# Optimization experiments

Hardware: AMD Instinct MI355X
Metric: run time of the kernel (lower is better)

The kernel has to match this reference:

```python
import jax, jax.numpy as jnp
import numpy as np

H = 512  # hidden_size
D = 512  # embed_dim == input_size
V = 50000  # embed_num
B, S = 64, 256
C = 5  # class_num


def setup_inputs() -> dict:
    key = jax.random.key(0)
    ks = jax.random.split(key, 8)
    sc_in = 1.0 / np.sqrt(D + H)
    return {
        "x": jax.random.randint(ks[0], (B, S), 0, V),
        "embed": jax.random.normal(ks[1], (V, D), dtype=jnp.float32) * 0.02,
        # gate order: [f, i, c, o]; each gate Linear(D+H -> H)
        "fwd_W": jax.random.normal(ks[2], (4, H, D + H), dtype=jnp.float32) * sc_in,
        "fwd_b": jax.random.normal(ks[3], (4, H), dtype=jnp.float32) * sc_in,
        "bwd_W": jax.random.normal(ks[4], (4, H, D + H), dtype=jnp.float32) * sc_in,
        "bwd_b": jax.random.normal(ks[5], (4, H), dtype=jnp.float32) * sc_in,
        "Wout": jax.random.normal(ks[6], (C, H), dtype=jnp.float32) * (1.0 / np.sqrt(H)),
        "bout": jax.random.normal(ks[7], (C,), dtype=jnp.float32) * 0.01,
    }


def _lstm_scan(xs, W, b):
    # xs: [S, B, D]; W: [4, H, D+H]; b: [4, H]
    Bsz = xs.shape[1]
    h0 = jnp.zeros((Bsz, H), xs.dtype)
    c0 = jnp.zeros((Bsz, H), xs.dtype)

    def step(carry, xt):
        h, c = carry
        z = jnp.concatenate([xt, h], axis=1)              # [B, D+H]
        gates = jnp.einsum('bk,ghk->gbh', z, W) + b[:, None, :]  # [4, B, H]
        f = jax.nn.sigmoid(gates[0])
        i = jax.nn.sigmoid(gates[1])
        ctil = jnp.tanh(gates[2])
        o = jax.nn.sigmoid(gates[3])
        # faithful to source: ct = f*ctil + i*ctil (prev cell state unused)
        c_new = (f + i) * ctil
        h_new = o * jnp.tanh(c_new)
        return (h_new, c_new), h_new

    _, hs = jax.lax.scan(step, (h0, c0), xs)
    return hs  # [S, B, H]


def reference(x, embed, fwd_W, fwd_b, bwd_W, bwd_b, Wout, bout):
    xe = embed[x]                      # [B, S, D]
    xs = jnp.transpose(xe, (1, 0, 2))  # [S, B, D]
    h_fwd = _lstm_scan(xs, fwd_W, fwd_b)                        # [S, B, H]
    h_bwd = _lstm_scan(xs[::-1], bwd_W, bwd_b)[::-1]            # aligned [S, B, H]
    combined = h_fwd * h_bwd           # elementwise product, per source
    pooled = jnp.max(jnp.tanh(combined), axis=0)  # max over time -> [B, H]
    return pooled @ Wout.T + bout      # [B, C]
```

## Files before the change

### kernel.cpp

```cpp
#include <hip/hip_runtime.h>
#include <math.h>

#define HH 512
#define DD 512
#define BB 64
#define SS 256
#define KK 1024
#define CC 5

typedef __attribute__((ext_vector_type(8))) short short8;
typedef __attribute__((ext_vector_type(4))) float float4v;

#define OFF_XEF     0u
#define OFF_HSPL    33554432u
#define OFF_FLG     34078720u
#define OFF_HIST    34079744u
#define OFF_POOLED  OFF_HSPL
#define HSPL_PLANE  131072

__device__ __forceinline__ unsigned f2bf_bits(float f) {
    unsigned u = __builtin_bit_cast(unsigned, f);
    return (u + 0x7fffu + ((u >> 16) & 1u)) >> 16;
}
__device__ __forceinline__ float sigm_(float v) {
    return 1.f / (1.f + expf(-v));
}
__device__ __forceinline__ float tanh_(float v) {
    return tanhf(v);
}

__global__ __launch_bounds__(256)
void gather_split_k(const int* __restrict__ x, const float* __restrict__ embed,
                    short* __restrict__ xef)
{
    const int s   = blockIdx.x;
    const int tid = threadIdx.x;
    const int b   = tid & 63;
    const int seg = tid >> 6;
    __shared__ int rows[BB];
    if (tid < BB) rows[tid] = x[tid * SS + s];
    __syncthreads();
    const float* e = embed + (size_t)rows[b] * DD + seg * 128;
    short* oh = xef + ((size_t)(s * 2 + 0) * BB + b) * 512 + seg * 128;
    short* ol = xef + ((size_t)(s * 2 + 1) * BB + b) * 512 + seg * 128;
    for (int k0 = 0; k0 < 128; k0 += 8) {
        const float4 a = *(const float4*)(e + k0);
        const float4 c = *(const float4*)(e + k0 + 4);
        const float ev[8] = {a.x, a.y, a.z, a.w, c.x, c.y, c.z, c.w};
        short8 vh, vl;
        #pragma unroll
        for (int j = 0; j < 8; ++j) {
            const unsigned hib = f2bf_bits(ev[j]);
            const float hif = __builtin_bit_cast(float, hib << 16);
            const unsigned lob = f2bf_bits(ev[j] - hif);
            vh[j] = (short)hib;
            vl[j] = (short)lob;
        }
        *(short8*)(oh + k0) = vh;
        *(short8*)(ol + k0) = vl;
    }
}

__global__ __launch_bounds__(256)
void zero_k(unsigned* __restrict__ base, int ndw)
{
    int i = blockIdx.x * 256 + threadIdx.x;
    const int stride = gridDim.x * 256;
    for (; i < ndw; i += stride) base[i] = 0u;
}

__global__ void __launch_bounds__(256, 1)
bilstm_recur_k(const short* __restrict__ xef,
               const float* __restrict__ fwd_W, const float* __restrict__ bwd_W,
               const float* __restrict__ fwd_b, const float* __restrict__ bwd_b,
               short* __restrict__ hspl, float* __restrict__ hist,
               unsigned* __restrict__ flg)
{
    extern __shared__ char smem[];
    short8* wlds = (short8*)smem;
    char*   hbuf = smem + 65536;
    float*  ex   = (float*)(smem + 131072);
    unsigned short* stg = (unsigned short*)(smem + 135168);

    const int w      = blockIdx.x;
    const int dir    = w >> 7;
    const int wlocal = w & 127;
    const int h0     = wlocal << 2;
    const int tid    = threadIdx.x;
    const int lane   = tid & 63;
    const int wv     = __builtin_amdgcn_readfirstlane(tid >> 6);
    const int n0     = wv << 4;
    const int nn     = lane & 15;
    const int quad   = lane >> 4;

    {
        const float* W = dir ? bwd_W : fwd_W;
        const int m  = lane & 15;
        const int g  = m >> 2;
        const int hh = m & 3;
        const float* wrow = W + ((size_t)g * HH + h0 + hh) * KK + quad * 8;
        for (int kk = 0; kk < 8; ++kk) {
            const int kt = wv * 8 + kk;
            const float4 a  = *(const float4*)(wrow + kt * 32);
            const float4 c4 = *(const float4*)(wrow + kt * 32 + 4);
            const float ev[8] = {a.x, a.y, a.z, a.w, c4.x, c4.y, c4.z, c4.w};
            short8 vh, vl;
            #pragma unroll
            for (int j = 0; j < 8; ++j) {
                const unsigned hib = f2bf_bits(ev[j]);
                const float hif = __builtin_bit_cast(float, hib << 16);
                const unsigned lob = f2bf_bits(ev[j] - hif);
                vh[j] = (short)hib;
                vl[j] = (short)lob;
            }
            wlds[(0 * 32 + kt) * 64 + lane] = vh;
            wlds[(1 * 32 + kt) * 64 + lane] = vl;
        }
    }
    __syncthreads();

    const float* bi = dir ? bwd_b : fwd_b;
    const float4 biasv = *(const float4*)(bi + quad * HH + h0);
    const float bias_arr[4] = {biasv.x, biasv.y, biasv.z, biasv.w};

    unsigned* myflg = flg + dir * 128;
    float* exw = ex + wv * 256;
    const int b = n0 + nn;
    const int h = h0 + quad;

    const int sb0 = tid >> 7;
    const int skb = (tid & 127) * 8;

    for (int t = 0; t < SS; ++t) {
        const int s = dir ? (SS - 1 - t) : t;
        const int p = t & 1;

        float4v acc = {0.f, 0.f, 0.f, 0.f};

        {
            const short8* xh8 = (const short8*)(xef +
                ((size_t)(s * 2 + 0) * BB + b) * 512 + quad * 8);
            const short8* xl8 = (const short8*)(xef +
                ((size_t)(s * 2 + 1) * BB + b) * 512 + quad * 8);
            #pragma unroll
            for (int kt = 0; kt < 16; ++kt) {
                const short8 xh  = xh8[kt * 4];
                const short8 xl  = xl8[kt * 4];
                const short8 whi = wlds[(0 * 32 + kt) * 64 + lane];
                const short8 wlo = wlds[(1 * 32 + kt) * 64 + lane];
                acc = __builtin_amdgcn_mfma_f32_16x16x32_bf16(whi, xh, acc, 0, 0, 0);
                acc = __builtin_amdgcn_mfma_f32_16x16x32_bf16(whi, xl, acc, 0, 0, 0);
                acc = __builtin_amdgcn_mfma_f32_16x16x32_bf16(wlo, xh, acc, 0, 0, 0);
            }
        }

        if (t > 0) {
            const unsigned tgt = (unsigned)t;
            unsigned va, vb;
            va = __hip_atomic_load(myflg + lane, __ATOMIC_RELAXED,
                                   __HIP_MEMORY_SCOPE_AGENT);
            vb = __hip_atomic_load(myflg + 64 + lane, __ATOMIC_RELAXED,
                                   __HIP_MEMORY_SCOPE_AGENT);
            while (__any(va < tgt || vb < tgt)) {
                __builtin_amdgcn_s_sleep(32);
                va = __hip_atomic_load(myflg + lane, __ATOMIC_RELAXED,
                                       __HIP_MEMORY_SCOPE_AGENT);
                vb = __hip_atomic_load(myflg + 64 + lane, __ATOMIC_RELAXED,
                                       __HIP_MEMORY_SCOPE_AGENT);
            }
            asm volatile("" ::: "memory");
        }

        {
            const unsigned long long* hq = (const unsigned long long*)
                ((const char*)hspl + (size_t)(p * 2 + dir) * 65536);
            const unsigned long long* lq = (const unsigned long long*)
                ((const char*)hspl + 262144 + (size_t)(p * 2 + dir) * 65536);

            unsigned long long sh[32], sl[32];
            #pragma unroll
            for (int it = 0; it < 32; ++it)
                sh[it] = __hip_atomic_load(hq + tid + it * 256, __ATOMIC_RELAXED,
                                           __HIP_MEMORY_SCOPE_AGENT);
            #pragma unroll
            for (int it = 0; it < 32; ++it)
                sl[it] = __hip_atomic_load(lq + tid + it * 256, __ATOMIC_RELAXED,
                                           __HIP_MEMORY_SCOPE_AGENT);

            #pragma unroll
            for (int it = 0; it < 32; ++it) {
                const int bb = sb0 + it * 2;
                *(unsigned long long*)(hbuf +
                    ((bb << 10) | (skb ^ ((bb & 7) << 4)))) = sh[it];
            }
            __syncthreads();
            #pragma unroll
            for (int kt = 0; kt < 16; ++kt) {
                const short8 uh = *(const short8*)(hbuf + ((b << 10) |
                    ((quad * 16 + kt * 64) ^ ((b & 7) << 4))));
                const short8 whi = wlds[(0 * 32 + 16 + kt) * 64 + lane];
                const short8 wlo = wlds[(1 * 32 + 16 + kt) * 64 + lane];
                acc = __builtin_amdgcn_mfma_f32_16x16x32_bf16(whi, uh, acc, 0, 0, 0);
                acc = __builtin_amdgcn_mfma_f32_16x16x32_bf16(wlo, uh, acc, 0, 0, 0);
            }
            __syncthreads();

            #pragma unroll
            for (int it = 0; it < 32; ++it) {
                const int bb = sb0 + it * 2;
                *(unsigned long long*)(hbuf +
                    ((bb << 10) | (skb ^ ((bb & 7) << 4)))) = sl[it];
            }
            __syncthreads();
            #pragma unroll
            for (int kt = 0; kt < 16; ++kt) {
                const short8 ul = *(const short8*)(hbuf + ((b << 10) |
                    ((quad * 16 + kt * 64) ^ ((b & 7) << 4))));
                const short8 whi = wlds[(0 * 32 + 16 + kt) * 64 + lane];
                acc = __builtin_amdgcn_mfma_f32_16x16x32_bf16(whi, ul, acc, 0, 0, 0);
            }
        }

        #pragma unroll
        for (int r2 = 0; r2 < 4; ++r2)
            exw[(quad * 4 + r2) * 16 + nn] = acc[r2] + bias_arr[r2];
        float pg[4];
        #pragma unroll
        for (int g_ = 0; g_ < 4; ++g_)
            pg[g_] = exw[(g_ * 4 + quad) * 16 + nn];

        const float f_  = sigm_(pg[0]);
        const float i_  = sigm_(pg[1]);
        const float ct  = tanh_(pg[2]);
        const float o_  = sigm_(pg[3]);
        const float c_  = (f_ + i_) * ct;
        const float hn  = o_ * tanh_(c_);

        const unsigned hib = f2bf_bits(hn);
        const float hif = __builtin_bit_cast(float, hib << 16);
        const unsigned lob = f2bf_bits(hn - hif);
        stg[(0 * 4 + quad) * 64 + b] = (unsigned short)hib;
        stg[(1 * 4 + quad) * 64 + b] = (unsigned short)lob;
        hist[(((size_t)dir * SS + s) * HH + h) * BB + b] = hn;
        __syncthreads();

        {
            const int plane = tid >> 7;
            const int d     = tid & 127;
            const int pb    = d >> 1;
            const int pair  = d & 1;
            const unsigned v0 = stg[(plane * 4 + pair * 2 + 0) * 64 + pb];
            const unsigned v1 = stg[(plane * 4 + pair * 2 + 1) * 64 + pb];
            const unsigned val = v0 | (v1 << 16);
            const size_t soff = ((size_t)((p ^ 1) * 2 + dir) * BB + pb) * HH
                                + h0 + pair * 2;
            unsigned* dst = (unsigned*)(hspl + (size_t)plane * HSPL_PLANE + soff);
            __hip_atomic_store(dst, val, __ATOMIC_RELAXED,
                               __HIP_MEMORY_SCOPE_AGENT);
        }
        asm volatile("s_waitcnt vmcnt(0)" ::: "memory");
        __syncthreads();
        if (tid == 0)
            __hip_atomic_store(myflg + wlocal, (unsigned)(t + 1),
                               __ATOMIC_RELAXED, __HIP_MEMORY_SCOPE_AGENT);
    }
}

__global__ __launch_bounds__(256)
void pool_k(const float* __restrict__ hist, float* __restrict__ pooled)
{
    const int i = blockIdx.x * 256 + threadIdx.x;
    float m = -2.0f;
    for (int s = 0; s < SS; ++s) {
        const float a = hist[(size_t)s * (HH * BB) + i];
        const float c = hist[(size_t)(SS + s) * (HH * BB) + i];
        m = fmaxf(m, tanhf(a * c));
    }
    pooled[i] = m;
}

__global__ __launch_bounds__(256)
void outgemm_k(const float* __restrict__ pooled, const float* __restrict__ Wout,
               const float* __restrict__ bout, float* __restrict__ out)
{
    const int c   = blockIdx.x;
    const int tid = threadIdx.x;
    const int b   = tid & 63;
    const int q   = __builtin_amdgcn_readfirstlane(tid >> 6);
    float p = 0.0f;
    for (int j = 0; j < 128; ++j) {
        const int h = q * 128 + j;
        p = fmaf(pooled[(size_t)h * BB + b], Wout[c * HH + h], p);
    }
    __shared__ float red[4][BB];
    red[q][b] = p;
    __syncthreads();
    if (tid < BB)
        out[tid * CC + c] = red[0][tid] + red[1][tid] + red[2][tid] + red[3][tid] + bout[c];
}

extern "C" void kernel_launch(void* const* d_in, const int* in_sizes, int n_in,
                              void* d_out, int out_size, void* d_ws, size_t ws_size,
                              hipStream_t stream)
{
    const int*   x     = (const int*)d_in[0];
    const float* embed = (const float*)d_in[1];
    const float* fwd_W = (const float*)d_in[2];
    const float* fwd_b = (const float*)d_in[3];
    const float* bwd_W = (const float*)d_in[4];
    const float* bwd_b = (const float*)d_in[5];
    const float* Wout  = (const float*)d_in[6];
    const float* bout  = (const float*)d_in[7];
    float* out = (float*)d_out;

    char* wsb = (char*)d_ws;
    short*    xef    = (short*)(wsb + OFF_XEF);
    short*    hspl   = (short*)(wsb + OFF_HSPL);
    unsigned* flg    = (unsigned*)(wsb + OFF_FLG);
    float*    hist   = (float*)(wsb + OFF_HIST);
    float*    pooled = (float*)(wsb + OFF_POOLED);

    gather_split_k<<<SS, 256, 0, stream>>>(x, embed, xef);
    zero_k<<<512, 256, 0, stream>>>((unsigned*)(wsb + OFF_HSPL),
                                    (int)((524288 + 1024) / 4));

    hipFuncSetAttribute((const void*)bilstm_recur_k,
                        hipFuncAttributeMaxDynamicSharedMemorySize, 136192);
    void* args[] = {(void*)&xef, (void*)&fwd_W, (void*)&bwd_W,
                    (void*)&fwd_b, (void*)&bwd_b,
                    (void*)&hspl, (void*)&hist, (void*)&flg};
    hipLaunchCooperativeKernel((void*)bilstm_recur_k, dim3(256), dim3(256),
                               args, 136192, stream);

    pool_k<<<128, 256, 0, stream>>>(hist, pooled);
    outgemm_k<<<CC, 256, 0, stream>>>(pooled, Wout, bout, out);
}
```

Before: 2.269 ms.

## Replace double-buffered h exchange with per-step rotating history slots

The hidden-state exchange buffer becomes a per-timestep history array: each step writes its split bf16 h into slot t+1 instead of alternating two buffers. This removes the separate fp32 hist store from the recurrent kernel, and the pool kernel now rebuilds h from the hi/lo bf16 planes. Reads switch from relaxed atomic 8-byte loads to plain 16-byte vector loads, which cuts instruction count on the serial critical path. The cost is a larger workspace, and the plain loads may be served from stale cache since the coherence guarantee of the atomic loads is gone.

New measurement: 2.147 ms. 1.06x faster.

```diff
diff --git a/kernel.cpp b/kernel.cpp
--- a/kernel.cpp
+++ b/kernel.cpp
@@ -12,11 +12,10 @@
 typedef __attribute__((ext_vector_type(4))) float float4v;
 
 #define OFF_XEF     0u
-#define OFF_HSPL    33554432u
-#define OFF_FLG     34078720u
-#define OFF_HIST    34079744u
-#define OFF_POOLED  OFF_HSPL
-#define HSPL_PLANE  131072
+#define OFF_ROT     33554432u
+#define ROT_SLOT_B  262144u
+#define OFF_FLG     100925440u
+#define OFF_POOLED  0u
 
 __device__ __forceinline__ unsigned f2bf_bits(float f) {
     unsigned u = __builtin_bit_cast(unsigned, f);
@@ -73,8 +72,7 @@
 bilstm_recur_k(const short* __restrict__ xef,
                const float* __restrict__ fwd_W, const float* __restrict__ bwd_W,
                const float* __restrict__ fwd_b, const float* __restrict__ bwd_b,
-               short* __restrict__ hspl, float* __restrict__ hist,
-               unsigned* __restrict__ flg)
+               short* __restrict__ rot, unsigned* __restrict__ flg)
 {
     extern __shared__ char smem[];
     short8* wlds = (short8*)smem;
@@ -126,14 +124,9 @@
     unsigned* myflg = flg + dir * 128;
     float* exw = ex + wv * 256;
     const int b = n0 + nn;
-    const int h = h0 + quad;
-
-    const int sb0 = tid >> 7;
-    const int skb = (tid & 127) * 8;
 
     for (int t = 0; t < SS; ++t) {
         const int s = dir ? (SS - 1 - t) : t;
-        const int p = t & 1;
 
         float4v acc = {0.f, 0.f, 0.f, 0.f};
 
@@ -172,26 +165,26 @@
         }
 
         {
-            const unsigned long long* hq = (const unsigned long long*)
-                ((const char*)hspl + (size_t)(p * 2 + dir) * 65536);
-            const unsigned long long* lq = (const unsigned long long*)
-                ((const char*)hspl + 262144 + (size_t)(p * 2 + dir) * 65536);
-
-            unsigned long long sh[32], sl[32];
-            #pragma unroll
-            for (int it = 0; it < 32; ++it)
-                sh[it] = __hip_atomic_load(hq + tid + it * 256, __ATOMIC_RELAXED,
-                                           __HIP_MEMORY_SCOPE_AGENT);
-            #pragma unroll
-            for (int it = 0; it < 32; ++it)
-                sl[it] = __hip_atomic_load(lq + tid + it * 256, __ATOMIC_RELAXED,
-                                           __HIP_MEMORY_SCOPE_AGENT);
-
-            #pragma unroll
-            for (int it = 0; it < 32; ++it) {
-                const int bb = sb0 + it * 2;
-                *(unsigned long long*)(hbuf +
-                    ((bb << 10) | (skb ^ ((bb & 7) << 4)))) = sh[it];
+            const char* slot = (const char*)rot + (size_t)t * ROT_SLOT_B
+                             + (size_t)dir * 65536;
+            const short8* hq = (const short8*)(slot);
+            const short8* lq = (const short8*)(slot + 131072);
+
+            short8 sh[16], sl[16];
+            #pragma unroll
+            for (int it = 0; it < 16; ++it)
+                sh[it] = hq[it * 256 + tid];
+            #pragma unroll
+            for (int it = 0; it < 16; ++it)
+                sl[it] = lq[it * 256 + tid];
+
+            const int kb = (tid & 63) * 16;
+            const int bbb = tid >> 6;
+
+            #pragma unroll
+            for (int it = 0; it < 16; ++it) {
+                const int bb = it * 4 + bbb;
+                *(short8*)(hbuf + ((bb << 10) | (kb ^ ((bb & 7) << 4)))) = sh[it];
             }
             __syncthreads();
             #pragma unroll
@@ -206,10 +199,9 @@
             __syncthreads();
 
             #pragma unroll
-            for (int it = 0; it < 32; ++it) {
-                const int bb = sb0 + it * 2;
-                *(unsigned long long*)(hbuf +
-                    ((bb << 10) | (skb ^ ((bb & 7) << 4)))) = sl[it];
+            for (int it = 0; it < 16; ++it) {
+                const int bb = it * 4 + bbb;
+                *(short8*)(hbuf + ((bb << 10) | (kb ^ ((bb & 7) << 4)))) = sl[it];
             }
             __syncthreads();
             #pragma unroll
@@ -241,7 +233,6 @@
         const unsigned lob = f2bf_bits(hn - hif);
         stg[(0 * 4 + quad) * 64 + b] = (unsigned short)hib;
         stg[(1 * 4 + quad) * 64 + b] = (unsigned short)lob;
-        hist[(((size_t)dir * SS + s) * HH + h) * BB + b] = hn;
         __syncthreads();
 
         {
@@ -252,9 +243,10 @@
             const unsigned v0 = stg[(plane * 4 + pair * 2 + 0) * 64 + pb];
             const unsigned v1 = stg[(plane * 4 + pair * 2 + 1) * 64 + pb];
             const unsigned val = v0 | (v1 << 16);
-            const size_t soff = ((size_t)((p ^ 1) * 2 + dir) * BB + pb) * HH
-                                + h0 + pair * 2;
-            unsigned* dst = (unsigned*)(hspl + (size_t)plane * HSPL_PLANE + soff);
+            const size_t so = (size_t)(t + 1) * 131072 + (size_t)plane * 65536
+                            + (size_t)dir * 32768 + (size_t)pb * 512
+                            + h0 + pair * 2;
+            unsigned* dst = (unsigned*)(rot + so);
             __hip_atomic_store(dst, val, __ATOMIC_RELAXED,
                                __HIP_MEMORY_SCOPE_AGENT);
         }
@@ -267,16 +259,27 @@
 }
 
 __global__ __launch_bounds__(256)
-void pool_k(const float* __restrict__ hist, float* __restrict__ pooled)
-{
-    const int i = blockIdx.x * 256 + threadIdx.x;
+void pool_k(const short* __restrict__ rot, float* __restrict__ pooled)
+{
+    const int tg = blockIdx.x * 256 + threadIdx.x;
+    const int b  = tg >> 9;
+    const int h  = tg & 511;
+    const int off = b * 512 + h;
     float m = -2.0f;
     for (int s = 0; s < SS; ++s) {
-        const float a = hist[(size_t)s * (HH * BB) + i];
-        const float c = hist[(size_t)(SS + s) * (HH * BB) + i];
-        m = fmaxf(m, tanhf(a * c));
-    }
-    pooled[i] = m;
+        const short* fs = rot + (size_t)(s + 1) * 131072;
+        const short* bs = rot + (size_t)(SS - s) * 131072;
+        const unsigned hf = (unsigned short)fs[off];
+        const unsigned lf = (unsigned short)fs[65536 + off];
+        const unsigned hb = (unsigned short)bs[32768 + off];
+        const unsigned lb = (unsigned short)bs[65536 + 32768 + off];
+        const float af = __builtin_bit_cast(float, hf << 16)
+                       + __builtin_bit_cast(float, lf << 16);
+        const float ab = __builtin_bit_cast(float, hb << 16)
+                       + __builtin_bit_cast(float, lb << 16);
+        m = fmaxf(m, tanhf(af * ab));
+    }
+    pooled[(size_t)h * BB + b] = m;
 }
 
 __global__ __launch_bounds__(256)
@@ -315,23 +318,23 @@
 
     char* wsb = (char*)d_ws;
     short*    xef    = (short*)(wsb + OFF_XEF);
-    short*    hspl   = (short*)(wsb + OFF_HSPL);
+    short*    rot    = (short*)(wsb + OFF_ROT);
     unsigned* flg    = (unsigned*)(wsb + OFF_FLG);
-    float*    hist   = (float*)(wsb + OFF_HIST);
     float*    pooled = (float*)(wsb + OFF_POOLED);
 
     gather_split_k<<<SS, 256, 0, stream>>>(x, embed, xef);
-    zero_k<<<512, 256, 0, stream>>>((unsigned*)(wsb + OFF_HSPL),
-                                    (int)((524288 + 1024) / 4));
+    zero_k<<<64, 256, 0, stream>>>((unsigned*)(wsb + OFF_ROT),
+                                   (int)(ROT_SLOT_B / 4));
+    zero_k<<<1, 256, 0, stream>>>(flg, 256);
 
     hipFuncSetAttribute((const void*)bilstm_recur_k,
                         hipFuncAttributeMaxDynamicSharedMemorySize, 136192);
     void* args[] = {(void*)&xef, (void*)&fwd_W, (void*)&bwd_W,
                     (void*)&fwd_b, (void*)&bwd_b,
-                    (void*)&hspl, (void*)&hist, (void*)&flg};
+                    (void*)&rot, (void*)&flg};
     hipLaunchCooperativeKernel((void*)bilstm_recur_k, dim3(256), dim3(256),
                                args, 136192, stream);
 
-    pool_k<<<128, 256, 0, stream>>>(hist, pooled);
+    pool_k<<<128, 256, 0, stream>>>(rot, pooled);
     outgemm_k<<<CC, 256, 0, stream>>>(pooled, Wout, bout, out);
 }
```
